# Optimization experiments

Measured on AMD Instinct MI355X. Metric: run time of the kernel, lower is better.

## Reference

```python
import jax, jax.numpy as jnp
import numpy as np

T, N, C, S = 1600, 32, 512, 200
BLANK = 0
ALPHA = 0.5
NEG = -1e30  # finite stand-in for -inf (safe for grads)


def setup_inputs() -> dict:
    key = jax.random.key(0)
    k1, k2, k3 = jax.random.split(key, 3)
    # valid log-probabilities (log-softmax over vocab), shape (T, N, C)
    log_probs = jax.nn.log_softmax(jax.random.normal(k1, (T, N, C), jnp.float32), axis=-1)
    # labels in [1, C) so blank=0 never appears in targets
    targets = jax.random.randint(k2, (N, S), 1, C)
    input_lens = jnp.full((N,), T, dtype=jnp.int32)
    target_lens = jax.random.randint(k3, (N,), S // 2, S + 1)
    return {"log_probs": log_probs, "targets": targets,
            "input_lens": input_lens, "target_lens": target_lens}


def _ctc_forward(log_probs, targets, input_lens, target_lens):
    """Per-example CTC negative log-likelihood (reduction='none')."""
    Tt, Nn, Cc = log_probs.shape
    Ss = targets.shape[1]
    L = 2 * Ss + 1  # extended label sequence: blank, l1, blank, l2, ...

    ext = jnp.zeros((Nn, L), dtype=targets.dtype).at[:, 1::2].set(targets)  # (N, L)
    s_idx = jnp.arange(L)
    ext_m2 = jnp.pad(ext, ((0, 0), (2, 0)), constant_values=BLANK)[:, :L]
    # skip transition s-2 -> s allowed only for non-blank labels differing from s-2
    allow_skip = (ext != BLANK) & (ext != ext_m2) & (s_idx >= 2)[None, :]

    emit0 = jnp.take_along_axis(log_probs[0], ext, axis=1)  # (N, L)
    alpha0 = jnp.full((Nn, L), NEG, jnp.float32)
    alpha0 = alpha0.at[:, 0].set(emit0[:, 0])
    alpha0 = alpha0.at[:, 1].set(jnp.where(target_lens >= 1, emit0[:, 1], NEG))

    def step(alpha, xs):
        lp_t, t = xs  # lp_t: (N, C)
        emit = jnp.take_along_axis(lp_t, ext, axis=1)  # (N, L)
        a1 = jnp.pad(alpha, ((0, 0), (1, 0)), constant_values=NEG)[:, :L]
        a2 = jnp.where(allow_skip,
                       jnp.pad(alpha, ((0, 0), (2, 0)), constant_values=NEG)[:, :L],
                       NEG)
        m = jnp.maximum(jnp.maximum(alpha, a1), a2)
        new = m + jnp.log(jnp.exp(alpha - m) + jnp.exp(a1 - m) + jnp.exp(a2 - m)) + emit
        active = (t < input_lens)[:, None]  # freeze trellis past input_len
        return jnp.where(active, new, alpha), None

    alpha, _ = jax.lax.scan(step, alpha0, (log_probs[1:], jnp.arange(1, Tt)))

    idx_last = (2 * target_lens).astype(jnp.int32)  # final blank position
    idx_prev = jnp.maximum(idx_last - 1, 0)  # final label position
    a_last = jnp.take_along_axis(alpha, idx_last[:, None], axis=1)[:, 0]
    a_prev = jnp.where(target_lens > 0,
                       jnp.take_along_axis(alpha, idx_prev[:, None], axis=1)[:, 0],
                       NEG)
    return -jnp.logaddexp(a_last, a_prev)  # (N,)


def reference(log_probs, targets, input_lens, target_lens):
    per_ex = _ctc_forward(log_probs, targets, input_lens, target_lens)
    # zero_infinity=True: zero out infeasible alignments
    per_ex = jnp.where(per_ex < 1e29, per_ex, 0.0)
    norm = jnp.maximum(target_lens.astype(jnp.float32), 1.0) ** ALPHA
    return jnp.mean(per_ex / norm)
```

## Files before the change

kernel.cpp:

```cpp
#include <hip/hip_runtime.h>

#define T_DIM 1600
#define N_DIM 32
#define C_DIM 512
#define S_DIM 200
#define RCP_LN2 1.44269504088896340736f
#define LN2F 0.69314718055994530942f
#define ESENT (-(1 << 28))

static __device__ __forceinline__ float fast_exp2(float x) {
#if __has_builtin(__builtin_amdgcn_exp2f)
    return __builtin_amdgcn_exp2f(x);
#else
    return exp2f(x);
#endif
}

static __device__ __forceinline__ float fast_log2(float x) {
#if __has_builtin(__builtin_amdgcn_logf)
    return __builtin_amdgcn_logf(x);
#else
    return log2f(x);
#endif
}

static __device__ __forceinline__ float dpp_shr1_f(float x) {
    return __int_as_float(__builtin_amdgcn_update_dpp(
        0, __float_as_int(x), 0x138, 0xf, 0xf, false));
}
static __device__ __forceinline__ int dpp_shr1_i(int x, int old0) {
    return __builtin_amdgcn_update_dpp(old0, x, 0x138, 0xf, 0xf, false);
}
static __device__ __forceinline__ int dpp_prefix_max_i(int x) {
    int t;
    t = __builtin_amdgcn_update_dpp(x, x, 0x111, 0xf, 0xf, false); x = (t > x) ? t : x;
    t = __builtin_amdgcn_update_dpp(x, x, 0x112, 0xf, 0xf, false); x = (t > x) ? t : x;
    t = __builtin_amdgcn_update_dpp(x, x, 0x114, 0xf, 0xf, false); x = (t > x) ? t : x;
    t = __builtin_amdgcn_update_dpp(x, x, 0x118, 0xf, 0xf, false); x = (t > x) ? t : x;
    t = __builtin_amdgcn_update_dpp(x, x, 0x142, 0xf, 0xf, false); x = (t > x) ? t : x;
    t = __builtin_amdgcn_update_dpp(x, x, 0x143, 0xf, 0xf, false); x = (t > x) ? t : x;
    return x;
}

static __device__ __forceinline__ void gl_lds16(const float* g, float* l) {
    __builtin_amdgcn_global_load_lds(
        (const __attribute__((address_space(1))) unsigned int*)g,
        (__attribute__((address_space(3))) unsigned int*)l, 16, 0, 0);
}

#define VMWAIT16() __builtin_amdgcn_s_waitcnt(0x4F70)
#define VMDRAIN()  __builtin_amdgcn_s_waitcnt(0x0F70)
#define SCHED0()   __builtin_amdgcn_sched_barrier(0)
#define PHASE_SYNC() do {                                                     \
        __builtin_amdgcn_sched_barrier(0);                                    \
        __builtin_amdgcn_s_waitcnt(0xC07F);              \
        __builtin_amdgcn_s_barrier();                                         \
        __builtin_amdgcn_sched_barrier(0);                                    \
    } while (0)

__global__ __launch_bounds__(192) void ctc_dp(
    const float* __restrict__ lp, const int* __restrict__ tgts,
    const int* __restrict__ input_lens, const int* __restrict__ target_lens,
    float* __restrict__ out, float* __restrict__ ws)
{
    __shared__ float rows[2][16][C_DIM];
    __shared__ float slab[2][5][16][64];

    const int blk = blockIdx.x;
    const int n = blk >> 1;
    const int role = blk & 1;
    const int tid = threadIdx.x;
    const int wid = tid >> 6;
    const int lane = tid & 63;
    const int* tgt = tgts + n * S_DIM;

    int len = input_lens[n];
    if (len > T_DIM) len = T_DIM;
    const int lenc = (len < 1) ? 1 : len;
    const int tl = target_lens[n];
    const int mid = (lenc + 1) >> 1;
    const int nsb = lenc - mid;
    const int nsteps = (role == 0) ? mid : nsb;
    const int nc = (nsteps + 15) >> 4;

    float* afin_g = ws + 96 + (size_t)n * 1152;
    float* bfin_g = afin_g + 512;
    int* escF_g = (int*)(afin_g + 1024);
    int* escB_g = escF_g + 64;
    int* counter = (int*)ws + n;
    int* arrivals = (int*)ws + 32;
    float* res = ws + 33;

    int lab[4];
    float skh[4];
    if (role == 0) {
#pragma unroll
        for (int jj = 0; jj < 4; ++jj) {
            int s = lane * 8 + 2 * jj + 1;
            int i = (s - 1) >> 1;
            int lb = 0;
            float al = 0.0f;
            if (i < S_DIM) {
                lb = tgt[i];
                if (s >= 3 && i >= 1) al = (tgt[i] != tgt[i - 1]) ? 1.0f : 0.0f;
            }
            if (lb < 0 || lb >= C_DIM) lb = 0;
            lab[jj] = lb;
            skh[jj] = al;
        }
    } else {
#pragma unroll
        for (int jj = 0; jj < 4; ++jj) {
            int shat = lane * 8 + 2 * jj + 1;
            int s = 510 - shat;
            int lb = 0;
            float al = 0.0f;
            if (s >= 1 && s <= 399) {
                lb = tgt[(s - 1) >> 1];
                if (s + 2 <= 400) al = (tgt[(s + 1) >> 1] != tgt[(s - 1) >> 1]) ? 1.0f : 0.0f;
            }
            if (lb < 0 || lb >= C_DIM) lb = 0;
            lab[jj] = lb;
            skh[jj] = al;
        }
    }

    const int r0 = (wid == 1) ? 0 : 8;

    auto tmap = [&](int ti) -> int {
        if (role == 0) return ti > mid - 1 ? mid - 1 : ti;
        int t = lenc - 1 - ti;
        return t < 0 ? 0 : t;
    };

#define STAGE(B_, c_) do {                                                    \
        _Pragma("unroll")                                                     \
        for (int rr_ = 0; rr_ < 8; ++rr_) {                                   \
            int r_ = r0 + rr_;                                                \
            int t_ = tmap((c_) * 16 + r_);                                    \
            const float* g_ = lp + ((size_t)t_ * N_DIM + n) * C_DIM + lane*4; \
            gl_lds16(g_,       &rows[(B_)][r_][0]);                           \
            gl_lds16(g_ + 256, &rows[(B_)][r_][256]);                         \
        }                                                                     \
    } while (0)

#define CONV(B_, S_) do {                                                     \
        float v_[40];                                                         \
        _Pragma("unroll")                                                     \
        for (int rr_ = 0; rr_ < 8; ++rr_) {                                   \
            int r_ = r0 + rr_;                                                \
            v_[rr_ * 5 + 0] = rows[(B_)][r_][0];                              \
            v_[rr_ * 5 + 1] = rows[(B_)][r_][lab[0]];                         \
            v_[rr_ * 5 + 2] = rows[(B_)][r_][lab[1]];                         \
            v_[rr_ * 5 + 3] = rows[(B_)][r_][lab[2]];                         \
            v_[rr_ * 5 + 4] = rows[(B_)][r_][lab[3]];                         \
        }                                                                     \
        __builtin_amdgcn_sched_barrier(0);                                    \
        _Pragma("unroll")                                                     \
        for (int rr_ = 0; rr_ < 8; ++rr_) {                                   \
            int r_ = r0 + rr_;                                                \
            _Pragma("unroll")                                                 \
            for (int j_ = 0; j_ < 5; ++j_)                                    \
                slab[(S_)][j_][r_][lane] =                                    \
                    fast_exp2(v_[rr_ * 5 + j_] * RCP_LN2);                    \
        }                                                                     \
    } while (0)

#define BOUNDARY() do {                                                       \
        float lm_ = fmaxf(fmaxf(fmaxf(a0, a1), fmaxf(a2, a3)),                \
                          fmaxf(fmaxf(a4, a5), fmaxf(a6, a7)));               \
        bool nz_ = (lm_ > 0.0f);                                              \
        int kl_ = (int)((__float_as_uint(lm_) >> 23) & 0xffu) - 127;          \
        int prop_ = nz_ ? (E + kl_) : ESENT;                                  \
        int g_ = dpp_prefix_max_i(prop_ + 32 * lane);                         \
        int Efin_ = g_ - 32 * lane;                                           \
        if (nz_) {                                                            \
            int sh_ = E - Efin_;                                              \
            int h1_ = sh_ / 2, h2_ = sh_ - h1_;                               \
            float f_ = fast_exp2((float)h1_), gg_ = fast_exp2((float)h2_);    \
            float fg_ = f_ * gg_;                                             \
            a0 *= fg_; a1 *= fg_; a2 *= fg_; a3 *= fg_;                       \
            a4 *= fg_; a5 *= fg_; a6 *= fg_; a7 *= fg_;                       \
        }                                                                     \
        int Eprev_ = dpp_shr1_i(Efin_, ESENT);                                \
        E = Efin_;                                                            \
        if (lane == 0) {                                                      \
            scale_d = 0.0f;                                                   \
        } else {                                                              \
            int d_ = Eprev_ - Efin_;               \
            scale_d = (d_ < -126) ? 0.0f : fast_exp2((float)d_);              \
        }                                                                     \
    } while (0)

#define GROUP_F(t0_, qb_, q_, FIRST_) do {                                    \
        _Pragma("unroll")                                                     \
        for (int r_ = 0; r_ < 8; ++r_) {                                      \
            int t_ = (t0_) + r_;                                              \
            if (t_ >= mid) break;                                             \
            float pb_ = q_[(qb_ + r_) * 5 + 0];                               \
            float p1_ = q_[(qb_ + r_) * 5 + 1];                               \
            float p3_ = q_[(qb_ + r_) * 5 + 2];                               \
            float p5_ = q_[(qb_ + r_) * 5 + 3];                               \
            float p7_ = q_[(qb_ + r_) * 5 + 4];                               \
            if ((FIRST_) && r_ == 0) {                                        \
                if (lane == 0) {                                              \
                    a0 = pb_;                                                 \
                    a1 = (tl >= 1) ? p1_ : 0.0f;                              \
                }                                                             \
            } else {                                                          \
                float P_ = dpp_shr1_f(a7) * scale_d;                          \
                float n0_ = (a0 + P_) * pb_;                                  \
                float n1_ = fmaf(skh[0], P_,  a1 + a0) * p1_;                 \
                float n2_ = (a2 + a1) * pb_;                                  \
                float n3_ = fmaf(skh[1], a1, a3 + a2) * p3_;                  \
                float n4_ = (a4 + a3) * pb_;                                  \
                float n5_ = fmaf(skh[2], a3, a5 + a4) * p5_;                  \
                float n6_ = (a6 + a5) * pb_;                                  \
                float n7_ = fmaf(skh[3], a5, a7 + a6) * p7_;                  \
                a0 = n0_; a1 = n1_; a2 = n2_; a3 = n3_;                       \
                a4 = n4_; a5 = n5_; a6 = n6_; a7 = n7_;                       \
            }                                                                 \
        }                                                                     \
    } while (0)

#define GROUP_B(i0_, qb_, q_) do {                                            \
        _Pragma("unroll")                                                     \
        for (int r_ = 0; r_ < 8; ++r_) {                                      \
            int ti_ = (i0_) + r_;                                             \
            if (ti_ >= nsb) break;                                            \
            float pb_ = q_[(qb_ + r_) * 5 + 0];                               \
            float p1_ = q_[(qb_ + r_) * 5 + 1];                               \
            float p3_ = q_[(qb_ + r_) * 5 + 2];                               \
            float p5_ = q_[(qb_ + r_) * 5 + 3];                               \
            float p7_ = q_[(qb_ + r_) * 5 + 4];                               \
            float c0_ = pb_ * a0, c1_ = p1_ * a1;                             \
            float c2_ = pb_ * a2, c3_ = p3_ * a3;                             \
            float c4_ = pb_ * a4, c5_ = p5_ * a5;                             \
            float c6_ = pb_ * a6, c7_ = p7_ * a7;                             \
            float P_ = dpp_shr1_f(c7_) * scale_d;                             \
            a0 = c0_ + P_;                                                    \
            a1 = fmaf(skh[0], P_,  c1_ + c0_);                                \
            a2 = c2_ + c1_;                                                   \
            a3 = fmaf(skh[1], c1_, c3_ + c2_);                                \
            a4 = c4_ + c3_;                                                   \
            a5 = fmaf(skh[2], c3_, c5_ + c4_);                                \
            a6 = c6_ + c5_;                                                   \
            a7 = fmaf(skh[3], c5_, c7_ + c6_);                                \
        }                                                                     \
    } while (0)

#define CONSUME(k_, S_, FIRST_) do {                                          \
        float q_[80];                                                         \
        _Pragma("unroll")                                                     \
        for (int r_ = 0; r_ < 16; ++r_)                                       \
            _Pragma("unroll")                                                 \
            for (int j_ = 0; j_ < 5; ++j_)                                    \
                q_[r_ * 5 + j_] = slab[(S_)][j_][r_][lane];                   \
        __builtin_amdgcn_sched_barrier(0);                                    \
        if (role == 0) {                                                      \
            GROUP_F((k_) * 16,     0, q_, FIRST_);                            \
            BOUNDARY();                                                       \
            GROUP_F((k_) * 16 + 8, 8, q_, false);                             \
            BOUNDARY();                                                       \
        } else {                                                              \
            GROUP_B((k_) * 16,     0, q_);                                    \
            BOUNDARY();                                                       \
            GROUP_B((k_) * 16 + 8, 8, q_);                                    \
            BOUNDARY();                                                       \
        }                                                                     \
    } while (0)

    if (wid >= 1) {
        STAGE(0, 0);
        STAGE(1, 1);
        VMWAIT16();
        CONV(0, 0);
    }
    PHASE_SYNC();

    float a0, a1, a2, a3, a4, a5, a6, a7;
    if (role == 0) {
        a0 = a1 = a2 = a3 = a4 = a5 = a6 = a7 = 0.0f;
    } else {
#define BINIT(aj_, j_) do {                                                   \
            int s_ = 510 - (lane * 8 + (j_));                                 \
            aj_ = (s_ == 2 * tl || (tl > 0 && s_ == 2 * tl - 1)) ? 1.0f : 0.0f; \
        } while (0)
        BINIT(a0, 0); BINIT(a1, 1); BINIT(a2, 2); BINIT(a3, 3);
        BINIT(a4, 4); BINIT(a5, 5); BINIT(a6, 6); BINIT(a7, 7);
#undef BINIT
    }
    int E = 0;
    float scale_d = (lane == 0) ? 0.0f : 1.0f;

    for (int k = 0; k < nc; ++k) {
        if (wid >= 1) {
            VMDRAIN();
            STAGE(k & 1, k + 2);
            CONV((k + 1) & 1, (k + 1) & 1);
        } else {
            CONSUME(k, k & 1, (k == 0));
        }
        PHASE_SYNC();
    }

    if (wid >= 1) {
        VMDRAIN();
        return;
    }

    {
        float4 lo = make_float4(a0, a1, a2, a3);
        float4 hi = make_float4(a4, a5, a6, a7);
        if (role == 0) {
            reinterpret_cast<float4*>(afin_g)[lane * 2] = lo;
            reinterpret_cast<float4*>(afin_g)[lane * 2 + 1] = hi;
            escF_g[lane] = E;
        } else {
            reinterpret_cast<float4*>(bfin_g)[lane * 2] = lo;
            reinterpret_cast<float4*>(bfin_g)[lane * 2 + 1] = hi;
            escB_g[lane] = E;
        }
    }

    __threadfence();
    int prev = 0;
    if (lane == 0)
        prev = __hip_atomic_fetch_add(counter, 1, __ATOMIC_ACQ_REL,
                                      __HIP_MEMORY_SCOPE_AGENT);
    prev = __shfl(prev, 0);
    if (prev != 1) return;

    __threadfence();

    {
        const int l = lane;
        const int Ef = escF_g[l];
        float m8 = -1e30f, s8 = 0.0f;
#pragma unroll
        for (int j = 0; j < 8; ++j) {
            int s = 8 * l + j;
            float x = -1e30f;
            if (s <= 400) {
                float af = afin_g[s];
                int shat = 510 - s;
                float bf = bfin_g[shat];
                if (af > 0.0f && bf > 0.0f)
                    x = fast_log2(af) + fast_log2(bf) + (float)(Ef + escB_g[shat >> 3]);
            }
            float m2 = fmaxf(m8, x);
            s8 = s8 * fast_exp2(m8 - m2) + fast_exp2(x - m2);
            m8 = m2;
        }
        float M = m8, V = s8;
#pragma unroll
        for (int off = 1; off < 64; off <<= 1) {
            float Mo = __shfl_xor(M, off);
            float Vo = __shfl_xor(V, off);
            float Mn = fmaxf(M, Mo);
            V = V * fast_exp2(M - Mn) + Vo * fast_exp2(Mo - Mn);
            M = Mn;
        }
        int prev2 = 0;
        if (lane == 0) {
            float X = M + fast_log2(V);
            float per_ex = -LN2F * X;
            if (!(per_ex < 1e29f)) per_ex = 0.0f;
            float tlf = (float)tl;
            if (tlf < 1.0f) tlf = 1.0f;
            res[n] = per_ex / sqrtf(tlf) * (1.0f / N_DIM);
            __threadfence();
            prev2 = __hip_atomic_fetch_add(arrivals, 1, __ATOMIC_ACQ_REL,
                                           __HIP_MEMORY_SCOPE_AGENT);
        }
        prev2 = __shfl(prev2, 0);
        if (prev2 == N_DIM - 1) {
            __threadfence();
            float v = (lane < N_DIM) ? res[lane] : 0.0f;
#pragma unroll
            for (int off = 1; off < 64; off <<= 1)
                v += __shfl_xor(v, off);
            if (lane == 0) out[0] = v;
        }
    }
#undef STAGE
#undef CONV
#undef BOUNDARY
#undef GROUP_F
#undef GROUP_B
#undef CONSUME
}

extern "C" void kernel_launch(void* const* d_in, const int* in_sizes, int n_in,
                              void* d_out, int out_size, void* d_ws, size_t ws_size,
                              hipStream_t stream) {
    (void)in_sizes; (void)n_in; (void)out_size; (void)ws_size;
    const float* lp   = (const float*)d_in[0];
    const int* tgts   = (const int*)d_in[1];
    const int* ilens  = (const int*)d_in[2];
    const int* tlens  = (const int*)d_in[3];

    hipMemsetAsync(d_ws, 0, 33 * sizeof(int), stream);
    ctc_dp<<<2 * N_DIM, 192, 0, stream>>>(lp, tgts, ilens, tlens,
                                          (float*)d_out, (float*)d_ws);
}
```

Measured before the change: 222.0 us.

## Triple-buffer staged rows, add producer waves, and pack slab as float4

Result: no change. 219.0 us (-1.3%).

```diff
diff --git a/kernel.cpp b/kernel.cpp
--- a/kernel.cpp
+++ b/kernel.cpp
@@ -48,7 +48,7 @@
         (__attribute__((address_space(3))) unsigned int*)l, 16, 0, 0);
 }
 
-#define VMWAIT16() __builtin_amdgcn_s_waitcnt(0x4F70)
+#define VMWAIT8()  __builtin_amdgcn_s_waitcnt(0x0F78)
 #define VMDRAIN()  __builtin_amdgcn_s_waitcnt(0x0F70)
 #define SCHED0()   __builtin_amdgcn_sched_barrier(0)
 #define PHASE_SYNC() do {                                                     \
@@ -58,13 +58,14 @@
         __builtin_amdgcn_sched_barrier(0);                                    \
     } while (0)
 
-__global__ __launch_bounds__(192) void ctc_dp(
+__global__ __launch_bounds__(320) void ctc_dp(
     const float* __restrict__ lp, const int* __restrict__ tgts,
     const int* __restrict__ input_lens, const int* __restrict__ target_lens,
     float* __restrict__ out, float* __restrict__ ws)
 {
-    __shared__ float rows[2][16][C_DIM];
-    __shared__ float slab[2][5][16][64];
+    __shared__ float rows[3][16][C_DIM];
+    __shared__ float4 slab4[2][16][64];
+    __shared__ float pbs[2][16];
 
     const int blk = blockIdx.x;
     const int n = blk >> 1;
@@ -125,7 +126,7 @@
         }
     }
 
-    const int r0 = (wid == 1) ? 0 : 8;
+    const int r0 = (wid - 1) * 4;
 
     auto tmap = [&](int ti) -> int {
         if (role == 0) return ti > mid - 1 ? mid - 1 : ti;
@@ -135,7 +136,7 @@
 
 #define STAGE(B_, c_) do {                                                    \
         _Pragma("unroll")                                                     \
-        for (int rr_ = 0; rr_ < 8; ++rr_) {                                   \
+        for (int rr_ = 0; rr_ < 4; ++rr_) {                                   \
             int r_ = r0 + rr_;                                                \
             int t_ = tmap((c_) * 16 + r_);                                    \
             const float* g_ = lp + ((size_t)t_ * N_DIM + n) * C_DIM + lane*4; \
@@ -145,9 +146,9 @@
     } while (0)
 
 #define CONV(B_, S_) do {                                                     \
-        float v_[40];                                                         \
-        _Pragma("unroll")                                                     \
-        for (int rr_ = 0; rr_ < 8; ++rr_) {                                   \
+        float v_[20];                                                         \
+        _Pragma("unroll")                                                     \
+        for (int rr_ = 0; rr_ < 4; ++rr_) {                                   \
             int r_ = r0 + rr_;                                                \
             v_[rr_ * 5 + 0] = rows[(B_)][r_][0];                              \
             v_[rr_ * 5 + 1] = rows[(B_)][r_][lab[0]];                         \
@@ -157,12 +158,15 @@
         }                                                                     \
         __builtin_amdgcn_sched_barrier(0);                                    \
         _Pragma("unroll")                                                     \
-        for (int rr_ = 0; rr_ < 8; ++rr_) {                                   \
+        for (int rr_ = 0; rr_ < 4; ++rr_) {                                   \
             int r_ = r0 + rr_;                                                \
-            _Pragma("unroll")                                                 \
-            for (int j_ = 0; j_ < 5; ++j_)                                    \
-                slab[(S_)][j_][r_][lane] =                                    \
-                    fast_exp2(v_[rr_ * 5 + j_] * RCP_LN2);                    \
+            float4 o_;                                                        \
+            o_.x = fast_exp2(v_[rr_ * 5 + 1] * RCP_LN2);                      \
+            o_.y = fast_exp2(v_[rr_ * 5 + 2] * RCP_LN2);                      \
+            o_.z = fast_exp2(v_[rr_ * 5 + 3] * RCP_LN2);                      \
+            o_.w = fast_exp2(v_[rr_ * 5 + 4] * RCP_LN2);                      \
+            slab4[(S_)][r_][lane] = o_;                                       \
+            if (lane == 0) pbs[(S_)][r_] = fast_exp2(v_[rr_ * 5 + 0] * RCP_LN2); \
         }                                                                     \
     } while (0)
 
@@ -192,16 +196,14 @@
         }                                                                     \
     } while (0)
 
-#define GROUP_F(t0_, qb_, q_, FIRST_) do {                                    \
+#define GROUP_F(t0_, qb_, q4_, pbv_, FIRST_) do {                             \
         _Pragma("unroll")                                                     \
         for (int r_ = 0; r_ < 8; ++r_) {                                      \
             int t_ = (t0_) + r_;                                              \
             if (t_ >= mid) break;                                             \
-            float pb_ = q_[(qb_ + r_) * 5 + 0];                               \
-            float p1_ = q_[(qb_ + r_) * 5 + 1];                               \
-            float p3_ = q_[(qb_ + r_) * 5 + 2];                               \
-            float p5_ = q_[(qb_ + r_) * 5 + 3];                               \
-            float p7_ = q_[(qb_ + r_) * 5 + 4];                               \
+            float pb_ = pbv_[qb_ + r_];                                       \
+            float p1_ = q4_[qb_ + r_].x, p3_ = q4_[qb_ + r_].y,               \
+                  p5_ = q4_[qb_ + r_].z, p7_ = q4_[qb_ + r_].w;               \
             if ((FIRST_) && r_ == 0) {                                        \
                 if (lane == 0) {                                              \
                     a0 = pb_;                                                 \
@@ -223,16 +225,14 @@
         }                                                                     \
     } while (0)
 
-#define GROUP_B(i0_, qb_, q_) do {                                            \
+#define GROUP_B(i0_, qb_, q4_, pbv_) do {                                     \
         _Pragma("unroll")                                                     \
         for (int r_ = 0; r_ < 8; ++r_) {                                      \
             int ti_ = (i0_) + r_;                                             \
             if (ti_ >= nsb) break;                                            \
-            float pb_ = q_[(qb_ + r_) * 5 + 0];                               \
-            float p1_ = q_[(qb_ + r_) * 5 + 1];                               \
-            float p3_ = q_[(qb_ + r_) * 5 + 2];                               \
-            float p5_ = q_[(qb_ + r_) * 5 + 3];                               \
-            float p7_ = q_[(qb_ + r_) * 5 + 4];                               \
+            float pb_ = pbv_[qb_ + r_];                                       \
+            float p1_ = q4_[qb_ + r_].x, p3_ = q4_[qb_ + r_].y,               \
+                  p5_ = q4_[qb_ + r_].z, p7_ = q4_[qb_ + r_].w;               \
             float c0_ = pb_ * a0, c1_ = p1_ * a1;                             \
             float c2_ = pb_ * a2, c3_ = p3_ * a3;                             \
             float c4_ = pb_ * a4, c5_ = p5_ * a5;                             \
@@ -250,22 +250,23 @@
     } while (0)
 
 #define CONSUME(k_, S_, FIRST_) do {                                          \
-        float q_[80];                                                         \
-        _Pragma("unroll")                                                     \
-        for (int r_ = 0; r_ < 16; ++r_)                                       \
-            _Pragma("unroll")                                                 \
-            for (int j_ = 0; j_ < 5; ++j_)                                    \
-                q_[r_ * 5 + j_] = slab[(S_)][j_][r_][lane];                   \
+        float4 q_[16];                                                        \
+        float pbq_[16];                                                       \
+        _Pragma("unroll")                                                     \
+        for (int r_ = 0; r_ < 16; ++r_) {                                     \
+            q_[r_] = slab4[(S_)][r_][lane];                                   \
+            pbq_[r_] = pbs[(S_)][r_];                                         \
+        }                                                                     \
         __builtin_amdgcn_sched_barrier(0);                                    \
         if (role == 0) {                                                      \
-            GROUP_F((k_) * 16,     0, q_, FIRST_);                            \
+            GROUP_F((k_) * 16,     0, q_, pbq_, FIRST_);                      \
             BOUNDARY();                                                       \
-            GROUP_F((k_) * 16 + 8, 8, q_, false);                             \
+            GROUP_F((k_) * 16 + 8, 8, q_, pbq_, false);                       \
             BOUNDARY();                                                       \
         } else {                                                              \
-            GROUP_B((k_) * 16,     0, q_);                                    \
+            GROUP_B((k_) * 16,     0, q_, pbq_);                              \
             BOUNDARY();                                                       \
-            GROUP_B((k_) * 16 + 8, 8, q_);                                    \
+            GROUP_B((k_) * 16 + 8, 8, q_, pbq_);                              \
             BOUNDARY();                                                       \
         }                                                                     \
     } while (0)
@@ -273,8 +274,9 @@
     if (wid >= 1) {
         STAGE(0, 0);
         STAGE(1, 1);
-        VMWAIT16();
+        VMWAIT8();
         CONV(0, 0);
+        STAGE(2, 2);
     }
     PHASE_SYNC();
 
@@ -295,9 +297,9 @@
 
     for (int k = 0; k < nc; ++k) {
         if (wid >= 1) {
-            VMDRAIN();
-            STAGE(k & 1, k + 2);
-            CONV((k + 1) & 1, (k + 1) & 1);
+            VMWAIT8();
+            CONV((k + 1) % 3, (k + 1) & 1);
+            STAGE((k + 3) % 3, k + 3);
         } else {
             CONSUME(k, k & 1, (k == 0));
         }
@@ -401,6 +403,6 @@
     const int* tlens  = (const int*)d_in[3];
 
     hipMemsetAsync(d_ws, 0, 33 * sizeof(int), stream);
-    ctc_dp<<<2 * N_DIM, 192, 0, stream>>>(lp, tgts, ilens, tlens,
+    ctc_dp<<<2 * N_DIM, 320, 0, stream>>>(lp, tgts, ilens, tlens,
                                           (float*)d_out, (float*)d_ws);
 }
```
